# Optimization experiments

Measured on AMD Instinct MI355X. Metric: run time of the kernel, lower is better.

The kernel has to match this reference:

```python
import jax, jax.numpy as jnp
import numpy as np

H, W, C = 56, 56, 192
WS, SS = 7, 3          # window_size, shift_size
NH, HD = 6, 32         # num_heads, head_dim
N = WS * WS            # tokens per window = 49
HIDDEN = 4 * C
EPS = 1e-5


def _rel_pos_index():
    coords = np.stack(np.meshgrid(np.arange(WS), np.arange(WS), indexing='ij'))  # (2,ws,ws)
    flat = coords.reshape(2, -1)
    rel = flat[:, :, None] - flat[:, None, :]            # (2,N,N)
    rel = rel.transpose(1, 2, 0)
    rel[:, :, 0] += WS - 1
    rel[:, :, 1] += WS - 1
    rel[:, :, 0] *= 2 * WS - 1
    return rel.sum(-1)                                   # (N,N) int


def _attn_mask():
    img = np.zeros((H, W))
    cnt = 0
    for hs in (slice(0, -WS), slice(-WS, -SS), slice(-SS, None)):
        for ws_ in (slice(0, -WS), slice(-WS, -SS), slice(-SS, None)):
            img[hs, ws_] = cnt
            cnt += 1
    mw = img.reshape(H // WS, WS, W // WS, WS).transpose(0, 2, 1, 3).reshape(-1, N)  # (nW,N)
    diff = mw[:, None, :] - mw[:, :, None]
    return np.where(diff != 0, -100.0, 0.0).astype(np.float32)  # (nW,N,N)


REL_IDX = jnp.asarray(_rel_pos_index())
ATTN_MASK = jnp.asarray(_attn_mask())


def _ln(x, w, b):
    mu = x.mean(-1, keepdims=True)
    var = ((x - mu) ** 2).mean(-1, keepdims=True)
    return (x - mu) * jax.lax.rsqrt(var + EPS) * w + b


def _window_partition(x):
    # (B,H,W,C) -> (B*nW, N, C)
    B = x.shape[0]
    x = x.reshape(B, H // WS, WS, W // WS, WS, C)
    x = x.transpose(0, 1, 3, 2, 4, 5)
    return x.reshape(-1, N, C)


def _window_reverse(win, B):
    # (B*nW, N, C) -> (B,H,W,C)
    x = win.reshape(B, H // WS, W // WS, WS, WS, C)
    x = x.transpose(0, 1, 3, 2, 4, 5)
    return x.reshape(B, H, W, C)


def setup_inputs() -> dict:
    key = jax.random.key(0)
    ks = jax.random.split(key, 16)
    s = 0.02
    return {
        'x': jax.random.normal(ks[0], (64, H * W, C), jnp.float32),
        'norm1_w': jnp.ones((C,), jnp.float32),
        'norm1_b': jnp.zeros((C,), jnp.float32),
        'qkv_w': jax.random.normal(ks[1], (C, 3 * C), jnp.float32) * s,
        'qkv_b': jnp.zeros((3 * C,), jnp.float32),
        'rpb': jax.random.normal(ks[2], ((2 * WS - 1) ** 2, NH), jnp.float32) * s,
        'proj_w': jax.random.normal(ks[3], (C, C), jnp.float32) * s,
        'proj_b': jnp.zeros((C,), jnp.float32),
        'norm2_w': jnp.ones((C,), jnp.float32),
        'norm2_b': jnp.zeros((C,), jnp.float32),
        'fc1_w': jax.random.normal(ks[4], (C, HIDDEN), jnp.float32) * s,
        'fc1_b': jnp.zeros((HIDDEN,), jnp.float32),
        'fc2_w': jax.random.normal(ks[5], (HIDDEN, C), jnp.float32) * s,
        'fc2_b': jnp.zeros((C,), jnp.float32),
    }


def reference(x, norm1_w, norm1_b, qkv_w, qkv_b, rpb, proj_w, proj_b,
              norm2_w, norm2_b, fc1_w, fc1_b, fc2_w, fc2_b):
    B = x.shape[0]
    nW = (H // WS) * (W // WS)
    shortcut = x
    h = _ln(x, norm1_w, norm1_b).reshape(B, H, W, C)
    # cyclic shift
    h = jnp.roll(h, shift=(-SS, -SS), axis=(1, 2))
    xw = _window_partition(h)                                   # (B*nW, N, C)
    # windowed MHA
    qkv = (xw @ qkv_w + qkv_b).reshape(-1, N, 3, NH, HD).transpose(2, 0, 3, 1, 4)
    q, k, v = qkv[0], qkv[1], qkv[2]                            # (Bn, NH, N, HD)
    scale = HD ** -0.5
    attn = jnp.einsum('bhnd,bhmd->bhnm', q * scale, k)          # (Bn, NH, N, N)
    bias = rpb[REL_IDX.reshape(-1)].reshape(N, N, NH).transpose(2, 0, 1)
    attn = attn + bias[None]
    attn = attn.reshape(B, nW, NH, N, N) + ATTN_MASK[None, :, None]
    attn = jax.nn.softmax(attn.reshape(-1, NH, N, N), axis=-1)
    out = jnp.einsum('bhnm,bhmd->bhnd', attn, v)
    out = out.transpose(0, 2, 1, 3).reshape(-1, N, C)
    out = out @ proj_w + proj_b
    # reverse windows + un-shift
    h = _window_reverse(out, B)
    h = jnp.roll(h, shift=(SS, SS), axis=(1, 2)).reshape(B, H * W, C)
    x = shortcut + h
    # MLP (exact GELU, as torch nn.GELU default)
    m = _ln(x, norm2_w, norm2_b)
    m = jax.nn.gelu(m @ fc1_w + fc1_b, approximate=False)
    m = m @ fc2_w + fc2_b
    return x + m
```

## Files before the change

### kernel.cpp

```cpp
#include <hip/hip_runtime.h>
#include <hip/hip_bf16.h>

typedef __hip_bfloat16 bf16;
typedef __attribute__((ext_vector_type(8))) short short8;
typedef __attribute__((ext_vector_type(4))) float floatx4;

__device__ __forceinline__ floatx4 mfma16(short8 a, short8 b, floatx4 c) {
  return __builtin_amdgcn_mfma_f32_16x16x32_bf16(a, b, c, 0, 0, 0);
}

__device__ __forceinline__ float wave_sum(float v) {
#pragma unroll
  for (int off = 1; off < 64; off <<= 1) v += __shfl_xor(v, off);
  return v;
}

__device__ __forceinline__ void gload16(const void* g, void* l) {
  __builtin_amdgcn_global_load_lds(
      (const __attribute__((address_space(1))) unsigned int*)g,
      (__attribute__((address_space(3))) unsigned int*)l, 16, 0, 0);
}

__device__ __forceinline__ short8 lds_frag(const char* base, int row, int kb) {
  return *(const short8*)(base + row * 384 + (kb ^ ((row & 7) << 4)));
}
__device__ __forceinline__ short8 lds_frag128(const char* base, int row, int kb) {
  return *(const short8*)(base + row * 128 + (kb ^ ((row & 7) << 4)));
}

__global__ __launch_bounds__(256) void k_wt(const float* __restrict__ w,
                                            bf16* __restrict__ wt, int K, int N) {
  int id = blockIdx.x * 256 + threadIdx.x;
  if (id < K * N) {
    int n = id / K;
    int k = id - n * K;
    wt[id] = __float2bfloat16(w[(long)k * N + n]);
  }
}

template <bool GATHER>
__global__ __launch_bounds__(256) void k_ln(const float* __restrict__ xin,
                                            const float* __restrict__ w,
                                            const float* __restrict__ b,
                                            bf16* __restrict__ out) {
  const int lane = threadIdx.x & 63;
  const long row = (long)blockIdx.x * 4 + (threadIdx.x >> 6);
  long srow;
  if (GATHER) {
    int win = (int)(row / 49);
    int token = (int)(row - (long)win * 49);
    int bimg = win >> 6, wi = (win & 63) >> 3, wj = win & 7;
    int ti = token / 7, tj = token - ti * 7;
    int h = wi * 7 + ti + 3; if (h >= 56) h -= 56;
    int ww = wj * 7 + tj + 3; if (ww >= 56) ww -= 56;
    srow = (long)bimg * 3136 + h * 56 + ww;
  } else {
    srow = row;
  }
  const float* src = xin + srow * 192;
  float v0 = src[lane], v1 = src[lane + 64], v2 = src[lane + 128];
  float mu = wave_sum(v0 + v1 + v2) * (1.f / 192.f);
  float d0 = v0 - mu, d1 = v1 - mu, d2 = v2 - mu;
  float var = wave_sum(d0 * d0 + d1 * d1 + d2 * d2) * (1.f / 192.f);
  float rs = rsqrtf(var + 1e-5f);
  bf16* dst = out + row * 192;
  dst[lane]       = __float2bfloat16(d0 * rs * w[lane] + b[lane]);
  dst[lane + 64]  = __float2bfloat16(d1 * rs * w[lane + 64] + b[lane + 64]);
  dst[lane + 128] = __float2bfloat16(d2 * rs * w[lane + 128] + b[lane + 128]);
}

template <int EPI>
__global__ __launch_bounds__(256, 3) void k_gemm(const bf16* __restrict__ A,
                                                 const bf16* __restrict__ Bt,
                                                 const float* __restrict__ bias,
                                                 bf16* __restrict__ Cbf,
                                                 float* __restrict__ Cfp,
                                                 const float* __restrict__ res,
                                                 int Ncols, int K, long row0) {
  __shared__ __align__(16) char As[64 * 384];
  __shared__ __align__(16) char Bs[64 * 384];
  const int t = threadIdx.x;
  const int lane = t & 63, wid = t >> 6;
  const int lanelo = lane & 15, quad = lane >> 4;
  const long m0 = (long)blockIdx.x * 64;
  const int n0 = blockIdx.y * 64;
  const int wm = (wid >> 1) * 32, wn = (wid & 1) * 32;

  floatx4 acc[2][2];
#pragma unroll
  for (int i = 0; i < 2; i++)
#pragma unroll
    for (int j = 0; j < 2; j++) acc[i][j] = (floatx4){0.f, 0.f, 0.f, 0.f};

  const char* Ab = (const char*)(A + m0 * (long)K);
  const char* Bb = (const char*)(Bt + (long)n0 * K);
  const int ldab = 2 * K;

  for (int k0b = 0; k0b < 2 * K; k0b += 384) {
    __syncthreads();
#pragma unroll
    for (int i = 0; i < 6; i++) {
      int c = i * 256 + t;
      int r = c / 24;
      int j = c - r * 24;
      int be = (j * 16) ^ ((r & 7) << 4);
      gload16(Ab + (long)r * ldab + k0b + be, As + c * 16);
      gload16(Bb + (long)r * ldab + k0b + be, Bs + c * 16);
    }
    __syncthreads();

#pragma unroll
    for (int kk = 0; kk < 6; kk++) {
      const int kb = kk * 64 + quad * 16;
      short8 a0 = lds_frag(As, wm + lanelo, kb);
      short8 a1 = lds_frag(As, wm + 16 + lanelo, kb);
      short8 b0 = lds_frag(Bs, wn + lanelo, kb);
      short8 b1 = lds_frag(Bs, wn + 16 + lanelo, kb);
      acc[0][0] = mfma16(a0, b0, acc[0][0]);
      acc[0][1] = mfma16(a0, b1, acc[0][1]);
      acc[1][0] = mfma16(a1, b0, acc[1][0]);
      acc[1][1] = mfma16(a1, b1, acc[1][1]);
    }
  }

#pragma unroll
  for (int mi = 0; mi < 2; mi++) {
#pragma unroll
    for (int reg = 0; reg < 4; reg++) {
      const long r = m0 + wm + mi * 16 + quad * 4 + reg;
      long orow = r;
      if (EPI == 2) {
        const long rg = row0 + r;
        int win = (int)(rg / 49);
        int token = (int)(rg - (long)win * 49);
        int bimg = win >> 6, wi = (win & 63) >> 3, wj = win & 7;
        int ti = token / 7, tj = token - ti * 7;
        int h = wi * 7 + ti + 3; if (h >= 56) h -= 56;
        int ww = wj * 7 + tj + 3; if (ww >= 56) ww -= 56;
        orow = (long)bimg * 3136 + h * 56 + ww;
      }
#pragma unroll
      for (int ni = 0; ni < 2; ni++) {
        const int c = n0 + wn + ni * 16 + lanelo;
        float v = acc[mi][ni][reg] + bias[c];
        if (EPI == 0) {
          Cbf[r * Ncols + c] = __float2bfloat16(v);
        } else if (EPI == 1) {
          v = 0.5f * v * (1.f + erff(v * 0.70710678118654752f));
          Cbf[r * Ncols + c] = __float2bfloat16(v);
        } else if (EPI == 2) {
          Cfp[orow * 192 + c] = v + res[orow * 192 + c];
        } else {
          Cfp[r * 192 + c] = v + res[r * 192 + c];
        }
      }
    }
  }
}

__global__ __launch_bounds__(256, 2) void k_mlp(float* xres,
                                                const float* __restrict__ lw,
                                                const float* __restrict__ lb,
                                                const bf16* __restrict__ w1t,
                                                const float* __restrict__ b1,
                                                const bf16* __restrict__ w2t,
                                                const float* __restrict__ b2) {
  __shared__ __align__(16) char As[64 * 384];
  __shared__ __align__(16) char B1s[64 * 384];
  __shared__ __align__(16) char B2s[192 * 128];
  __shared__ __align__(16) char Hs[64 * 128];
  const int t = threadIdx.x, lane = t & 63, wid = t >> 6;
  const int lanelo = lane & 15, quad = lane >> 4;
  const long row0 = (long)blockIdx.x * 64;
  const int wm = (wid >> 1) * 32;
  const int wn = (wid & 1) * 32;
  const int wn2 = (wid & 1) * 96;

  for (int i = 0; i < 16; i++) {
    int r = wid * 16 + i;
    const float* src = xres + (row0 + r) * 192;
    float v0 = src[lane], v1 = src[lane + 64], v2 = src[lane + 128];
    float mu = wave_sum(v0 + v1 + v2) * (1.f / 192.f);
    float d0 = v0 - mu, d1 = v1 - mu, d2 = v2 - mu;
    float var = wave_sum(d0 * d0 + d1 * d1 + d2 * d2) * (1.f / 192.f);
    float rs = rsqrtf(var + 1e-5f);
    int sw = (r & 7) << 4;
    *(bf16*)(As + r * 384 + ((2 * lane) ^ sw)) =
        __float2bfloat16(d0 * rs * lw[lane] + lb[lane]);
    *(bf16*)(As + r * 384 + ((128 + 2 * lane) ^ sw)) =
        __float2bfloat16(d1 * rs * lw[lane + 64] + lb[lane + 64]);
    *(bf16*)(As + r * 384 + ((256 + 2 * lane) ^ sw)) =
        __float2bfloat16(d2 * rs * lw[lane + 128] + lb[lane + 128]);
  }

  floatx4 acc2[2][6];
#pragma unroll
  for (int mi = 0; mi < 2; mi++)
#pragma unroll
    for (int ni = 0; ni < 6; ni++) acc2[mi][ni] = (floatx4){0.f, 0.f, 0.f, 0.f};

  for (int nc = 0; nc < 12; nc++) {
#pragma unroll
    for (int i = 0; i < 6; i++) {
      int c = i * 256 + t;
      int r1 = c / 24, j1 = c - r1 * 24;
      gload16((const char*)w1t + (long)(nc * 64 + r1) * 384 +
                  ((j1 * 16) ^ ((r1 & 7) << 4)),
              B1s + c * 16);
      int r2 = c >> 3, j2 = c & 7;
      gload16((const char*)w2t + (long)r2 * 1536 + nc * 128 +
                  ((j2 * 16) ^ ((r2 & 7) << 4)),
              B2s + c * 16);
    }
    __syncthreads();

    floatx4 acc1[2][2];
#pragma unroll
    for (int mi = 0; mi < 2; mi++)
#pragma unroll
      for (int ni = 0; ni < 2; ni++) acc1[mi][ni] = (floatx4){0.f, 0.f, 0.f, 0.f};
#pragma unroll
    for (int kk = 0; kk < 6; kk++) {
      const int kb = kk * 64 + quad * 16;
      short8 a0 = lds_frag(As, wm + lanelo, kb);
      short8 a1 = lds_frag(As, wm + 16 + lanelo, kb);
      short8 b0 = lds_frag(B1s, wn + lanelo, kb);
      short8 b1f = lds_frag(B1s, wn + 16 + lanelo, kb);
      acc1[0][0] = mfma16(a0, b0, acc1[0][0]);
      acc1[0][1] = mfma16(a0, b1f, acc1[0][1]);
      acc1[1][0] = mfma16(a1, b0, acc1[1][0]);
      acc1[1][1] = mfma16(a1, b1f, acc1[1][1]);
    }

#pragma unroll
    for (int ni = 0; ni < 2; ni++) {
      const int cl = wn + ni * 16 + lanelo;
      const float b1v = b1[nc * 64 + cl];
#pragma unroll
      for (int mi = 0; mi < 2; mi++)
#pragma unroll
        for (int reg = 0; reg < 4; reg++) {
          int r = wm + mi * 16 + quad * 4 + reg;
          float v = acc1[mi][ni][reg] + b1v;
          v = 0.5f * v * (1.f + erff(v * 0.70710678118654752f));
          *(bf16*)(Hs + r * 128 + ((2 * cl) ^ ((r & 7) << 4))) =
              __float2bfloat16(v);
        }
    }
    __syncthreads();

#pragma unroll
    for (int ks = 0; ks < 2; ks++) {
      const int kb = ks * 64 + quad * 16;
      short8 ha0 = lds_frag128(Hs, wm + lanelo, kb);
      short8 ha1 = lds_frag128(Hs, wm + 16 + lanelo, kb);
#pragma unroll
      for (int ni = 0; ni < 6; ni++) {
        short8 bv = lds_frag128(B2s, wn2 + ni * 16 + lanelo, kb);
        acc2[0][ni] = mfma16(ha0, bv, acc2[0][ni]);
        acc2[1][ni] = mfma16(ha1, bv, acc2[1][ni]);
      }
    }
    __syncthreads();
  }

#pragma unroll
  for (int mi = 0; mi < 2; mi++)
#pragma unroll
    for (int ni = 0; ni < 6; ni++) {
      const int c = wn2 + ni * 16 + lanelo;
      const float b2v = b2[c];
#pragma unroll
      for (int reg = 0; reg < 4; reg++) {
        const long g = (row0 + wm + mi * 16 + quad * 4 + reg) * 192 + c;
        xres[g] = acc2[mi][ni][reg] + b2v + xres[g];
      }
    }
}

__global__ __launch_bounds__(256, 2) void k_attn(const bf16* __restrict__ qkv,
                                                 const float* __restrict__ rpb,
                                                 bf16* __restrict__ out) {
  __shared__ __align__(16) bf16 smem[4 * 7424];
  const int t = threadIdx.x, lane = t & 63, wid = t >> 6;
  const int lanelo = lane & 15, quad = lane >> 4;
  const int unit = blockIdx.x * 4 + wid;
  const int win = unit / 6, head = unit - win * 6;
  bf16* Qs = smem + wid * 7424;
  bf16* Ks = Qs + 2560;
  bf16* Vt = Qs + 5120;
  bf16* Ps = Qs;
  const long rowbase = (long)win * 49;
  const bf16* base = qkv + rowbase * 576 + head * 32;

  for (int idx = lane; idx < 196; idx += 64) {
    int tok = idx >> 2, ch = (idx & 3) * 8;
    *(uint4*)(&Qs[tok * 40 + ch]) = *(const uint4*)(base + (long)tok * 576 + ch);
    *(uint4*)(&Ks[tok * 40 + ch]) = *(const uint4*)(base + (long)tok * 576 + 192 + ch);
    union { uint4 u; bf16 h[8]; } tv;
    tv.u = *(const uint4*)(base + (long)tok * 576 + 384 + ch);
#pragma unroll
    for (int jj = 0; jj < 8; jj++) Vt[(ch + jj) * 72 + tok] = tv.h[jj];
  }
  for (int idx = lane; idx < 480; idx += 64) {
    int d = idx / 15, c = 49 + (idx - d * 15);
    Vt[d * 72 + c] = __float2bfloat16(0.f);
  }
  __syncthreads();

  floatx4 aS[4][4];
#pragma unroll
  for (int mi = 0; mi < 4; mi++)
#pragma unroll
    for (int ni = 0; ni < 4; ni++) aS[mi][ni] = (floatx4){0.f, 0.f, 0.f, 0.f};
  {
    short8 aq[4], bk[4];
#pragma unroll
    for (int mi = 0; mi < 4; mi++)
      aq[mi] = *(const short8*)(&Qs[(mi * 16 + lanelo) * 40 + quad * 8]);
#pragma unroll
    for (int ni = 0; ni < 4; ni++)
      bk[ni] = *(const short8*)(&Ks[(ni * 16 + lanelo) * 40 + quad * 8]);
#pragma unroll
    for (int mi = 0; mi < 4; mi++)
#pragma unroll
      for (int ni = 0; ni < 4; ni++) aS[mi][ni] = mfma16(aq[mi], bk[ni], aS[mi][ni]);
  }

  const int w_in = win & 63, wiw = w_in >> 3, wjw = w_in & 7;
  int cTi[4], cTj[4], cLab[4];
  bool cval[4];
#pragma unroll
  for (int ni = 0; ni < 4; ni++) {
    int j = ni * 16 + lanelo;
    cval[ni] = (j < 49);
    if (j > 48) j = 48;
    int ti = j / 7, tj = j - ti * 7;
    int rr = wiw * 7 + ti, cc = wjw * 7 + tj;
    cTi[ni] = ti;
    cTj[ni] = tj;
    cLab[ni] = ((rr < 49) ? 0 : (rr < 53 ? 1 : 2)) * 3 +
               ((cc < 49) ? 0 : (cc < 53 ? 1 : 2));
  }

  const float scale = 0.17677669529663687f;
  float rinv[16];
#pragma unroll
  for (int mi = 0; mi < 4; mi++) {
#pragma unroll
    for (int reg = 0; reg < 4; reg++) {
      int i = mi * 16 + quad * 4 + reg;
      if (i > 48) i = 48;
      int ti = i / 7, tj = i - ti * 7;
      int rr = wiw * 7 + ti, cc = wjw * 7 + tj;
      int rlab = ((rr < 49) ? 0 : (rr < 53 ? 1 : 2)) * 3 +
                 ((cc < 49) ? 0 : (cc < 53 ? 1 : 2));
      float sv[4];
      float mx = -1e30f;
#pragma unroll
      for (int ni = 0; ni < 4; ni++) {
        float s;
        if (cval[ni]) {
          int ridx = (ti - cTi[ni] + 6) * 13 + (tj - cTj[ni] + 6);
          float bb = rpb[ridx * 6 + head];
          if (rlab != cLab[ni]) bb -= 100.f;
          s = aS[mi][ni][reg] * scale + bb;
        } else {
          s = -1e30f;
        }
        sv[ni] = s;
        mx = fmaxf(mx, s);
      }
      mx = fmaxf(mx, __shfl_xor(mx, 1));
      mx = fmaxf(mx, __shfl_xor(mx, 2));
      mx = fmaxf(mx, __shfl_xor(mx, 4));
      mx = fmaxf(mx, __shfl_xor(mx, 8));
      float sum = 0.f;
#pragma unroll
      for (int ni = 0; ni < 4; ni++) {
        float p = __expf(sv[ni] - mx);
        sv[ni] = p;
        sum += p;
      }
      sum += __shfl_xor(sum, 1);
      sum += __shfl_xor(sum, 2);
      sum += __shfl_xor(sum, 4);
      sum += __shfl_xor(sum, 8);
      rinv[mi * 4 + reg] = 1.f / sum;
#pragma unroll
      for (int ni = 0; ni < 4; ni++) aS[mi][ni][reg] = sv[ni];
    }
  }
  __syncthreads();

#pragma unroll
  for (int mi = 0; mi < 4; mi++)
#pragma unroll
    for (int ni = 0; ni < 4; ni++)
#pragma unroll
      for (int reg = 0; reg < 4; reg++) {
        int i = mi * 16 + quad * 4 + reg, j = ni * 16 + lanelo;
        Ps[i * 72 + j] = __float2bfloat16(aS[mi][ni][reg]);
      }
  __syncthreads();

  floatx4 aO[4][2];
#pragma unroll
  for (int mi = 0; mi < 4; mi++)
#pragma unroll
    for (int ni = 0; ni < 2; ni++) aO[mi][ni] = (floatx4){0.f, 0.f, 0.f, 0.f};
#pragma unroll
  for (int k0 = 0; k0 < 64; k0 += 32) {
    short8 ap[4], bv[2];
#pragma unroll
    for (int mi = 0; mi < 4; mi++)
      ap[mi] = *(const short8*)(&Ps[(mi * 16 + lanelo) * 72 + k0 + quad * 8]);
#pragma unroll
    for (int ni = 0; ni < 2; ni++)
      bv[ni] = *(const short8*)(&Vt[(ni * 16 + lanelo) * 72 + k0 + quad * 8]);
#pragma unroll
    for (int mi = 0; mi < 4; mi++)
#pragma unroll
      for (int ni = 0; ni < 2; ni++) aO[mi][ni] = mfma16(ap[mi], bv[ni], aO[mi][ni]);
  }

#pragma unroll
  for (int mi = 0; mi < 4; mi++)
#pragma unroll
    for (int reg = 0; reg < 4; reg++) {
      int i = mi * 16 + quad * 4 + reg;
      if (i < 49) {
        float rv = rinv[mi * 4 + reg];
#pragma unroll
        for (int ni = 0; ni < 2; ni++) {
          int d = ni * 16 + lanelo;
          out[(rowbase + i) * 192 + head * 32 + d] =
              __float2bfloat16(aO[mi][ni][reg] * rv);
        }
      }
    }
}

extern "C" void kernel_launch(void* const* d_in, const int* in_sizes, int n_in,
                              void* d_out, int out_size, void* d_ws, size_t ws_size,
                              hipStream_t stream) {
  const float* x     = (const float*)d_in[0];
  const float* n1w   = (const float*)d_in[1];
  const float* n1b   = (const float*)d_in[2];
  const float* qkvw  = (const float*)d_in[3];
  const float* qkvb  = (const float*)d_in[4];
  const float* rpb   = (const float*)d_in[5];
  const float* projw = (const float*)d_in[6];
  const float* projb = (const float*)d_in[7];
  const float* n2w   = (const float*)d_in[8];
  const float* n2b   = (const float*)d_in[9];
  const float* fc1w  = (const float*)d_in[10];
  const float* fc1b  = (const float*)d_in[11];
  const float* fc2w  = (const float*)d_in[12];
  const float* fc2b  = (const float*)d_in[13];
  float* outf = (float*)d_out;

  const long CR = 50176;
  const int  NCH = 4;

  char* ws = (char*)d_ws;
  bf16* xw      = (bf16*)(ws + 0);
  bf16* qkvC    = (bf16*)(ws + 77070336LL);
  bf16* attC    = (bf16*)(ws + 134873088LL);
  bf16* wt_qkv  = (bf16*)(ws + 154140672LL);
  bf16* wt_proj = (bf16*)(ws + 154140672LL + 221184LL);
  bf16* wt_fc1  = (bf16*)(ws + 154140672LL + 294912LL);
  bf16* wt_fc2  = (bf16*)(ws + 154140672LL + 589824LL);

  k_wt<<<dim3((192 * 576 + 255) / 256), 256, 0, stream>>>(qkvw, wt_qkv, 192, 576);
  k_wt<<<dim3((192 * 192 + 255) / 256), 256, 0, stream>>>(projw, wt_proj, 192, 192);
  k_wt<<<dim3((192 * 768 + 255) / 256), 256, 0, stream>>>(fc1w, wt_fc1, 192, 768);
  k_wt<<<dim3((768 * 192 + 255) / 256), 256, 0, stream>>>(fc2w, wt_fc2, 768, 192);

  k_ln<true><<<dim3(50176), 256, 0, stream>>>(x, n1w, n1b, xw);

  for (int c = 0; c < NCH; c++) {
    const long r0 = c * CR;
    k_gemm<0><<<dim3(784, 9), 256, 0, stream>>>(xw + r0 * 192, wt_qkv, qkvb,
                                                qkvC, nullptr, nullptr, 576, 192, 0);
    k_attn<<<dim3(1536), 256, 0, stream>>>(qkvC, rpb, attC);
    k_gemm<2><<<dim3(784, 3), 256, 0, stream>>>(attC, wt_proj, projb, nullptr,
                                                outf, x, 192, 192, r0);
  }

  k_mlp<<<dim3(3136), 256, 0, stream>>>(outf, n2w, n2b, wt_fc1, fc1b,
                                        wt_fc2, fc2b);
}
```

Measured before the change: 1.015 ms.

## Enlarge MLP block to 128 rows and register-prefetch weight chunks

The fused MLP kernel now handles 128 rows per block with 512 threads instead of 64 rows with 256, so each staged weight chunk serves twice as many rows. The asynchronous global-to-LDS weight loads are replaced by register prefetching, where the next chunk's weights are loaded into registers while the current chunk is computed. The visible hunks leave the LayerNorm loop at 16 rows per wave and the fc1/fc2 MFMA tiling unchanged, so correctness depends on the hidden code being updated to cover 8 waves. The doubled LDS use and the extra registers allow only one block per CU, which lowers occupancy.

```diff
diff --git a/kernel.cpp b/kernel.cpp
--- a/kernel.cpp
+++ b/kernel.cpp
@@ -158,23 +158,40 @@
   }
 }
 
-__global__ __launch_bounds__(256, 2) void k_mlp(float* xres,
+__global__ __launch_bounds__(512, 1) void k_mlp(float* xres,
                                                 const float* __restrict__ lw,
                                                 const float* __restrict__ lb,
                                                 const bf16* __restrict__ w1t,
                                                 const float* __restrict__ b1,
                                                 const bf16* __restrict__ w2t,
                                                 const float* __restrict__ b2) {
-  __shared__ __align__(16) char As[64 * 384];
+  __shared__ __align__(16) char As[128 * 384];
   __shared__ __align__(16) char B1s[64 * 384];
   __shared__ __align__(16) char B2s[192 * 128];
-  __shared__ __align__(16) char Hs[64 * 128];
+  __shared__ __align__(16) char Hs[128 * 128];
   const int t = threadIdx.x, lane = t & 63, wid = t >> 6;
   const int lanelo = lane & 15, quad = lane >> 4;
-  const long row0 = (long)blockIdx.x * 64;
+  const long row0 = (long)blockIdx.x * 128;
   const int wm = (wid >> 1) * 32;
   const int wn = (wid & 1) * 32;
   const int wn2 = (wid & 1) * 96;
+
+  int c1r[3], c1j[3], c2r[3], c2j[3];
+#pragma unroll
+  for (int i = 0; i < 3; i++) {
+    int c = i * 512 + t;
+    c1r[i] = c / 24; c1j[i] = c - c1r[i] * 24;
+    c2r[i] = c >> 3; c2j[i] = c & 7;
+  }
+
+  uint4 w1r[3], w2r[3];
+#pragma unroll
+  for (int i = 0; i < 3; i++) {
+    w1r[i] = *(const uint4*)((const char*)w1t + (long)c1r[i] * 384 +
+                             ((c1j[i] * 16) ^ ((c1r[i] & 7) << 4)));
+    w2r[i] = *(const uint4*)((const char*)w2t + (long)c2r[i] * 1536 +
+                             ((c2j[i] * 16) ^ ((c2r[i] & 7) << 4)));
+  }
 
   for (int i = 0; i < 16; i++) {
     int r = wid * 16 + i;
@@ -201,16 +218,19 @@
 
   for (int nc = 0; nc < 12; nc++) {
 #pragma unroll
-    for (int i = 0; i < 6; i++) {
-      int c = i * 256 + t;
-      int r1 = c / 24, j1 = c - r1 * 24;
-      gload16((const char*)w1t + (long)(nc * 64 + r1) * 384 +
-                  ((j1 * 16) ^ ((r1 & 7) << 4)),
-              B1s + c * 16);
-      int r2 = c >> 3, j2 = c & 7;
-      gload16((const char*)w2t + (long)r2 * 1536 + nc * 128 +
-                  ((j2 * 16) ^ ((r2 & 7) << 4)),
-              B2s + c * 16);
+    for (int i = 0; i < 3; i++) {
+      *(uint4*)(B1s + (i * 512 + t) * 16) = w1r[i];
+      *(uint4*)(B2s + (i * 512 + t) * 16) = w2r[i];
+    }
+    {
+      const int ncn = (nc < 11) ? nc + 1 : 11;
+#pragma unroll
+      for (int i = 0; i < 3; i++) {
+        w1r[i] = *(const uint4*)((const char*)w1t + (long)(ncn * 64 + c1r[i]) * 384 +
+                                 ((c1j[i] * 16) ^ ((c1r[i] & 7) << 4)));
+        w2r[i] = *(const uint4*)((const char*)w2t + (long)c2r[i] * 1536 + ncn * 128 +
+                                 ((c2j[i] * 16) ^ ((c2r[i] & 7) << 4)));
+      }
     }
     __syncthreads();
 
@@ -488,6 +508,6 @@
                                                 outf, x, 192, 192, r0);
   }
 
-  k_mlp<<<dim3(3136), 256, 0, stream>>>(outf, n2w, n2b, wt_fc1, fc1b,
+  k_mlp<<<dim3(1568), 512, 0, stream>>>(outf, n2w, n2b, wt_fc1, fc1b,
                                         wt_fc2, fc2b);
 }
```

Result: slower. 1.048 ms (+3.2%).

## Stream MLP weights from global into registers, drop weight LDS staging

Applied to the files above, without the earlier changes.

The fused MLP kernel stops staging fc1/fc2 weight tiles in shared memory. Each wave now reads its B fragments directly from global memory (likely L2-resident) and covers all 64 rows with a 16-column slice of the hidden chunk. The hidden activations are double-buffered in LDS, so only one barrier per chunk is needed. Cutting LDS use and raising launch bounds to 3 blocks per SM are meant to increase occupancy and remove barrier stalls, at the cost of uncoalesced per-lane global loads with latency exposed on the MFMA path.

```diff
diff --git a/kernel.cpp b/kernel.cpp
--- a/kernel.cpp
+++ b/kernel.cpp
@@ -158,7 +158,7 @@
   }
 }
 
-__global__ __launch_bounds__(256, 2) void k_mlp(float* xres,
+__global__ __launch_bounds__(256, 3) void k_mlp(float* xres,
                                                 const float* __restrict__ lw,
                                                 const float* __restrict__ lb,
                                                 const bf16* __restrict__ w1t,
@@ -166,15 +166,10 @@
                                                 const bf16* __restrict__ w2t,
                                                 const float* __restrict__ b2) {
   __shared__ __align__(16) char As[64 * 384];
-  __shared__ __align__(16) char B1s[64 * 384];
-  __shared__ __align__(16) char B2s[192 * 128];
-  __shared__ __align__(16) char Hs[64 * 128];
+  __shared__ __align__(16) char Hs[2][64 * 128];
   const int t = threadIdx.x, lane = t & 63, wid = t >> 6;
   const int lanelo = lane & 15, quad = lane >> 4;
   const long row0 = (long)blockIdx.x * 64;
-  const int wm = (wid >> 1) * 32;
-  const int wn = (wid & 1) * 32;
-  const int wn2 = (wid & 1) * 96;
 
   for (int i = 0; i < 16; i++) {
     int r = wid * 16 + i;
@@ -193,86 +188,75 @@
         __float2bfloat16(d2 * rs * lw[lane + 128] + lb[lane + 128]);
   }
 
-  floatx4 acc2[2][6];
-#pragma unroll
-  for (int mi = 0; mi < 2; mi++)
-#pragma unroll
-    for (int ni = 0; ni < 6; ni++) acc2[mi][ni] = (floatx4){0.f, 0.f, 0.f, 0.f};
+  floatx4 acc2[4][3];
+#pragma unroll
+  for (int mi = 0; mi < 4; mi++)
+#pragma unroll
+    for (int ni = 0; ni < 3; ni++) acc2[mi][ni] = (floatx4){0.f, 0.f, 0.f, 0.f};
+
+  __syncthreads();
+
+  const int hcol = wid * 16 + lanelo;
+  const int ocol0 = wid * 48;
 
   for (int nc = 0; nc < 12; nc++) {
-#pragma unroll
-    for (int i = 0; i < 6; i++) {
-      int c = i * 256 + t;
-      int r1 = c / 24, j1 = c - r1 * 24;
-      gload16((const char*)w1t + (long)(nc * 64 + r1) * 384 +
-                  ((j1 * 16) ^ ((r1 & 7) << 4)),
-              B1s + c * 16);
-      int r2 = c >> 3, j2 = c & 7;
-      gload16((const char*)w2t + (long)r2 * 1536 + nc * 128 +
-                  ((j2 * 16) ^ ((r2 & 7) << 4)),
-              B2s + c * 16);
-    }
-    __syncthreads();
-
-    floatx4 acc1[2][2];
-#pragma unroll
-    for (int mi = 0; mi < 2; mi++)
-#pragma unroll
-      for (int ni = 0; ni < 2; ni++) acc1[mi][ni] = (floatx4){0.f, 0.f, 0.f, 0.f};
+    const char* w1p = (const char*)w1t + (long)(nc * 64 + hcol) * 384;
+    floatx4 acc1[4];
+#pragma unroll
+    for (int mi = 0; mi < 4; mi++) acc1[mi] = (floatx4){0.f, 0.f, 0.f, 0.f};
 #pragma unroll
     for (int kk = 0; kk < 6; kk++) {
       const int kb = kk * 64 + quad * 16;
-      short8 a0 = lds_frag(As, wm + lanelo, kb);
-      short8 a1 = lds_frag(As, wm + 16 + lanelo, kb);
-      short8 b0 = lds_frag(B1s, wn + lanelo, kb);
-      short8 b1f = lds_frag(B1s, wn + 16 + lanelo, kb);
-      acc1[0][0] = mfma16(a0, b0, acc1[0][0]);
-      acc1[0][1] = mfma16(a0, b1f, acc1[0][1]);
-      acc1[1][0] = mfma16(a1, b0, acc1[1][0]);
-      acc1[1][1] = mfma16(a1, b1f, acc1[1][1]);
-    }
-
-#pragma unroll
-    for (int ni = 0; ni < 2; ni++) {
-      const int cl = wn + ni * 16 + lanelo;
-      const float b1v = b1[nc * 64 + cl];
-#pragma unroll
-      for (int mi = 0; mi < 2; mi++)
-#pragma unroll
-        for (int reg = 0; reg < 4; reg++) {
-          int r = wm + mi * 16 + quad * 4 + reg;
-          float v = acc1[mi][ni][reg] + b1v;
-          v = 0.5f * v * (1.f + erff(v * 0.70710678118654752f));
-          *(bf16*)(Hs + r * 128 + ((2 * cl) ^ ((r & 7) << 4))) =
-              __float2bfloat16(v);
-        }
-    }
+      short8 bf = *(const short8*)(w1p + kb);
+#pragma unroll
+      for (int mi = 0; mi < 4; mi++) {
+        short8 af = lds_frag(As, mi * 16 + lanelo, kb);
+        acc1[mi] = mfma16(af, bf, acc1[mi]);
+      }
+    }
+
+    char* H = Hs[nc & 1];
+    const float b1v = b1[nc * 64 + hcol];
+#pragma unroll
+    for (int mi = 0; mi < 4; mi++)
+#pragma unroll
+      for (int reg = 0; reg < 4; reg++) {
+        int r = mi * 16 + quad * 4 + reg;
+        float v = acc1[mi][reg] + b1v;
+        v = 0.5f * v * (1.f + erff(v * 0.70710678118654752f));
+        *(bf16*)(H + r * 128 + ((2 * hcol) ^ ((r & 7) << 4))) =
+            __float2bfloat16(v);
+      }
     __syncthreads();
 
 #pragma unroll
     for (int ks = 0; ks < 2; ks++) {
       const int kb = ks * 64 + quad * 16;
-      short8 ha0 = lds_frag128(Hs, wm + lanelo, kb);
-      short8 ha1 = lds_frag128(Hs, wm + 16 + lanelo, kb);
-#pragma unroll
-      for (int ni = 0; ni < 6; ni++) {
-        short8 bv = lds_frag128(B2s, wn2 + ni * 16 + lanelo, kb);
-        acc2[0][ni] = mfma16(ha0, bv, acc2[0][ni]);
-        acc2[1][ni] = mfma16(ha1, bv, acc2[1][ni]);
-      }
-    }
-    __syncthreads();
-  }
-
-#pragma unroll
-  for (int mi = 0; mi < 2; mi++)
-#pragma unroll
-    for (int ni = 0; ni < 6; ni++) {
-      const int c = wn2 + ni * 16 + lanelo;
+      short8 ha[4];
+#pragma unroll
+      for (int mi = 0; mi < 4; mi++)
+        ha[mi] = lds_frag128(H, mi * 16 + lanelo, kb);
+#pragma unroll
+      for (int ni = 0; ni < 3; ni++) {
+        short8 bv = *(const short8*)((const char*)w2t +
+                                     (long)(ocol0 + ni * 16 + lanelo) * 1536 +
+                                     nc * 128 + kb);
+#pragma unroll
+        for (int mi = 0; mi < 4; mi++)
+          acc2[mi][ni] = mfma16(ha[mi], bv, acc2[mi][ni]);
+      }
+    }
+  }
+
+#pragma unroll
+  for (int mi = 0; mi < 4; mi++)
+#pragma unroll
+    for (int ni = 0; ni < 3; ni++) {
+      const int c = ocol0 + ni * 16 + lanelo;
       const float b2v = b2[c];
 #pragma unroll
       for (int reg = 0; reg < 4; reg++) {
-        const long g = (row0 + wm + mi * 16 + quad * 4 + reg) * 192 + c;
+        const long g = (row0 + mi * 16 + quad * 4 + reg) * 192 + c;
         xres[g] = acc2[mi][ni][reg] + b2v + xres[g];
       }
     }
```

After: 1.020 ms. Within noise of the previous version (+0.5%).
